# Optimization experiments

Hardware: AMD Instinct MI355X
Metric: run time of the kernel (lower is better)

## Reference

```python
import jax, jax.numpy as jnp
import numpy as np

B, L_I, L_H, L_Q, Hs, Ws, K, A = 256, 2, 150, 10, 128, 128, 40, 5


def _conv(x, w, pad):
    # NCHW conv, stride 1
    return jax.lax.conv_general_dilated(
        x, w, window_strides=(1, 1), padding=[(pad, pad), (pad, pad)],
        dimension_numbers=('NCHW', 'OIHW', 'NCHW'))


def setup_inputs() -> dict:
    key = jax.random.key(0)
    ks = jax.random.split(key, 8)
    return {
        'input_view': jax.random.normal(ks[0], (B, L_I, Hs, Ws), dtype=jnp.float32),
        'coords': jax.random.randint(ks[1], (B, 4), 0, Hs, dtype=jnp.int32),
        'h_w': jax.random.normal(ks[2], (L_H, L_I, 3, 3), dtype=jnp.float32) * 0.05,
        'h_b': jax.random.normal(ks[3], (L_H,), dtype=jnp.float32) * 0.05,
        'r_w': jax.random.normal(ks[4], (1, L_H, 1, 1), dtype=jnp.float32) * 0.05,
        'q_w': jax.random.normal(ks[5], (L_Q, 1, 3, 3), dtype=jnp.float32) * 0.05,
        'w': jax.random.normal(ks[6], (L_Q, 1, 3, 3), dtype=jnp.float32) * 0.05,
        'fc_w': jax.random.normal(ks[7], (A, L_Q), dtype=jnp.float32) * 0.05,
    }


def reference(input_view, coords, h_w, h_b, r_w, q_w, w, fc_w):
    # process_input: h = Conv3x3(input_view), r = Conv1x1(h), q0 = Conv3x3(r)
    h = _conv(input_view, h_w, pad=1) + h_b[None, :, None, None]
    r = _conv(h, r_w, pad=0)                       # [B,1,H,W] reward map
    q = _conv(r, q_w, pad=1)                       # [B,L_Q,H,W]
    v = jnp.max(q, axis=1, keepdims=True)          # [B,1,H,W]

    # value_iteration: k-1 sweeps of eval_q + channel max, then one final eval_q
    wq = jnp.concatenate([q_w, w], axis=1)         # [L_Q,2,3,3]

    def step(_, v):
        q_i = _conv(jnp.concatenate([r, v], axis=1), wq, pad=1)
        return jnp.max(q_i, axis=1, keepdims=True)

    v = jax.lax.fori_loop(0, K - 1, step, v)
    q = _conv(jnp.concatenate([r, v], axis=1), wq, pad=1)  # [B,L_Q,H,W]

    # get_action: gather q at agent state, then fc (no bias)
    sx, sy = coords[:, 0], coords[:, 1]
    q_out = q[jnp.arange(B), :, sx, sy]            # [B,L_Q]
    logits = q_out @ fc_w.T                        # [B,5]
    return logits
```

## Files before the change

kernel.cpp:

```cpp
#include <hip/hip_runtime.h>

#define NBATCH 256
#define LI 2
#define LH 150
#define LQ 10
#define HS 128
#define WSD 128
#define KIT 40
#define AOUT 5

#define LCOLS 132
#define LROWS 130
#define PLANE (LROWS * LCOLS)
#define LDS_DWORDS (2 * PLANE)

typedef float v2f __attribute__((ext_vector_type(2)));

__global__ void prep_weff(const float* __restrict__ h_w,
                          const float* __restrict__ h_b,
                          const float* __restrict__ r_w,
                          float* __restrict__ w_eff) {
  const int t = threadIdx.x;
  if (t < 18) {
    const int i = t / 9, k = t % 9;
    double s = 0.0;
    for (int h = 0; h < LH; ++h)
      s += (double)r_w[h] * (double)h_w[(h * LI + i) * 9 + k];
    w_eff[t] = (float)s;
  } else if (t == 18) {
    double s = 0.0;
    for (int h = 0; h < LH; ++h)
      s += (double)r_w[h] * (double)h_b[h];
    w_eff[18] = (float)s;
  }
}


#define LOAD_PROW(P, R, W)                                                   \
  {                                                                          \
    const float4 b_ = *reinterpret_cast<const float4*>((P) + (R) * LCOLS);   \
    const float2 c_ = *reinterpret_cast<const float2*>((P) + (R) * LCOLS + 4); \
    W[0] = (v2f){b_.x, b_.y};                                                \
    W[1] = (v2f){b_.z, b_.w};                                                \
    W[2] = (v2f){c_.x, c_.y};                                                \
  }

#define TAPROW(KY, WARR, K0, K1, K2)                                         \
    a0 = __builtin_elementwise_fma((v2f){(K0), (K0)}, WARR[KY][0], a0);      \
    a1 = __builtin_elementwise_fma((v2f){(K0), (K0)}, WARR[KY][1], a1);      \
    a0.x = __builtin_fmaf((K1), WARR[KY][0].y, a0.x);                        \
    a0.y = __builtin_fmaf((K1), WARR[KY][1].x, a0.y);                        \
    a1.x = __builtin_fmaf((K1), WARR[KY][1].y, a1.x);                        \
    a1.y = __builtin_fmaf((K1), WARR[KY][2].x, a1.y);                        \
    a0 = __builtin_elementwise_fma((v2f){(K2), (K2)}, WARR[KY][1], a0);      \
    a1 = __builtin_elementwise_fma((v2f){(K2), (K2)}, WARR[KY][2], a1);

#define VI_CH(QC, WC, MERGE)                                                 \
  {                                                                          \
    const float* qc = (QC);                                                  \
    const float* wc = (WC);                                                  \
    v2f a0 = (v2f){qc[0], qc[0]} * rw[0][0];                                 \
    v2f a1 = (v2f){qc[0], qc[0]} * rw[0][1];                                 \
    a0.x = __builtin_fmaf(qc[1], rw[0][0].y, a0.x);                          \
    a0.y = __builtin_fmaf(qc[1], rw[0][1].x, a0.y);                          \
    a1.x = __builtin_fmaf(qc[1], rw[0][1].y, a1.x);                          \
    a1.y = __builtin_fmaf(qc[1], rw[0][2].x, a1.y);                          \
    a0 = __builtin_elementwise_fma((v2f){qc[2], qc[2]}, rw[0][1], a0);       \
    a1 = __builtin_elementwise_fma((v2f){qc[2], qc[2]}, rw[0][2], a1);       \
    TAPROW(1, rw, qc[3], qc[4], qc[5])                                       \
    TAPROW(2, rw, qc[6], qc[7], qc[8])                                       \
    TAPROW(0, vw, wc[0], wc[1], wc[2])                                       \
    TAPROW(1, vw, wc[3], wc[4], wc[5])                                       \
    TAPROW(2, vw, wc[6], wc[7], wc[8])                                       \
    MERGE                                                                    \
  }

#define VI_ROW(DY)                                                           \
  {                                                                          \
    v2f o0, o1;                                                              \
    VI_CH(q_w, w_in, o0 = a0; o1 = a1;)                                      \
    _Pragma("unroll 3")                                                      \
    for (int c = 1; c < LQ; ++c) {                                           \
      VI_CH(q_w + c * 9, w_in + c * 9,                                       \
            o0 = __builtin_elementwise_max(o0, a0);                          \
            o1 = __builtin_elementwise_max(o1, a1);)                         \
    }                                                                        \
    outv[DY][0] = o0; outv[DY][1] = o1;                                      \
  }

#define WIN_SHIFT2(NEXTROW)                                                  \
  {                                                                          \
    _Pragma("unroll")                                                        \
    for (int j = 0; j < 3; ++j) {                                            \
      rw[0][j] = rw[1][j]; rw[1][j] = rw[2][j];                              \
      vw[0][j] = vw[1][j]; vw[1][j] = vw[2][j];                              \
    }                                                                        \
    LOAD_PROW(rp, (NEXTROW), rw[2])                                          \
    LOAD_PROW(vp, (NEXTROW), vw[2])                                          \
  }

#define R_ROW(DY)                                                            \
  {                                                                          \
    v2f a0 = (v2f){beff, beff};                                              \
    v2f a1 = a0;                                                             \
    TAPROW(0, rw, w_eff[0], w_eff[1], w_eff[2])                              \
    TAPROW(1, rw, w_eff[3], w_eff[4], w_eff[5])                              \
    TAPROW(2, rw, w_eff[6], w_eff[7], w_eff[8])                              \
    TAPROW(0, vw, w_eff[9], w_eff[10], w_eff[11])                            \
    TAPROW(1, vw, w_eff[12], w_eff[13], w_eff[14])                           \
    TAPROW(2, vw, w_eff[15], w_eff[16], w_eff[17])                           \
    racc[DY][0] = a0; racc[DY][1] = a1;                                      \
  }

__global__ __launch_bounds__(1024)
__attribute__((amdgpu_waves_per_eu(4, 4)))
void vin_main(const float* __restrict__ input,
              const int* __restrict__ coords,
              const float* __restrict__ q_w,
              const float* __restrict__ w_in,
              const float* __restrict__ fc_w,
              const float* __restrict__ w_eff,
              float* __restrict__ out) {
  extern __shared__ float lds[];
  float* rplane = lds;
  float* vplane = lds + PLANE;

  const int b = blockIdx.x;
  const int tid = threadIdx.x;
  const int ty = tid >> 5;
  const int tx = tid & 31;
  const int y0 = ty << 2;
  const int x0 = tx << 2;
  const int nb_base = y0 * LCOLS + x0;
  const int wrow0 = (y0 + 1) * LCOLS + x0;

  for (int i = tid; i < LDS_DWORDS; i += 1024) lds[i] = 0.0f;
  __syncthreads();

  const float* in0 = input + (size_t)b * (LI * HS * WSD);
  const float* in1 = in0 + HS * WSD;
  {
    const float4* in40 = (const float4*)in0;
    const float4* in41 = (const float4*)in1;
    for (int i = tid; i < HS * WSD / 4; i += 1024) {
      const int y = i >> 5, x4 = (i & 31) << 2;
      const float4 a = in40[i];
      const float4 c = in41[i];
      float* r_ = rplane + (y + 1) * LCOLS + x4;
      float* v_ = vplane + (y + 1) * LCOLS + x4;
      r_[1] = a.x; r_[2] = a.y; r_[3] = a.z; r_[4] = a.w;
      v_[1] = c.x; v_[2] = c.y; v_[3] = c.z; v_[4] = c.w;
    }
  }
  __syncthreads();

  {
    const float* rp = rplane + nb_base;
    const float* vp = vplane + nb_base;
    v2f rw[3][3], vw[3][3], racc[4][2];
    LOAD_PROW(rp, 0, rw[0]) LOAD_PROW(rp, 1, rw[1]) LOAD_PROW(rp, 2, rw[2])
    LOAD_PROW(vp, 0, vw[0]) LOAD_PROW(vp, 1, vw[1]) LOAD_PROW(vp, 2, vw[2])
    const float beff = w_eff[18];
    R_ROW(0) WIN_SHIFT2(3) R_ROW(1) WIN_SHIFT2(4) R_ROW(2) WIN_SHIFT2(5) R_ROW(3)
    __syncthreads();
#pragma unroll
    for (int dy = 0; dy < 4; ++dy) {
      float* r_ = rplane + wrow0 + dy * LCOLS;
      float* v_ = vplane + wrow0 + dy * LCOLS;
      r_[1] = racc[dy][0].x; r_[2] = racc[dy][0].y;
      r_[3] = racc[dy][1].x; r_[4] = racc[dy][1].y;
      v_[1] = 0.0f; v_[2] = 0.0f; v_[3] = 0.0f; v_[4] = 0.0f;
    }
  }
  __syncthreads();

#pragma unroll 1
  for (int it = 0; it < KIT; ++it) {
    const float* rp = rplane + nb_base;
    const float* vp = vplane + nb_base;
    v2f rw[3][3], vw[3][3], outv[4][2];
    LOAD_PROW(rp, 0, rw[0]) LOAD_PROW(rp, 1, rw[1]) LOAD_PROW(rp, 2, rw[2])
    LOAD_PROW(vp, 0, vw[0]) LOAD_PROW(vp, 1, vw[1]) LOAD_PROW(vp, 2, vw[2])
    VI_ROW(0) WIN_SHIFT2(3) VI_ROW(1) WIN_SHIFT2(4) VI_ROW(2) WIN_SHIFT2(5) VI_ROW(3)
    __syncthreads();
#pragma unroll
    for (int dy = 0; dy < 4; ++dy) {
      float* v_ = vplane + wrow0 + dy * LCOLS;
      v_[1] = outv[dy][0].x; v_[2] = outv[dy][0].y;
      v_[3] = outv[dy][1].x; v_[4] = outv[dy][1].y;
    }
    __syncthreads();
  }

  if (tid == 0) {
    const int sx = coords[b * 4 + 0];
    const int sy = coords[b * 4 + 1];
    float qv[LQ];
#pragma unroll 1
    for (int c = 0; c < LQ; ++c) {
      float s = 0.0f;
#pragma unroll
      for (int kk = 0; kk < 9; ++kk) {
        const int ky = kk / 3, kx = kk % 3;
        const int off = (sx + ky) * LCOLS + (sy + kx);
        s = __builtin_fmaf(q_w[c * 9 + kk], rplane[off],
            __builtin_fmaf(w_in[c * 9 + kk], vplane[off], s));
      }
      qv[c] = s;
    }
#pragma unroll 1
    for (int a = 0; a < AOUT; ++a) {
      float s = 0.0f;
#pragma unroll
      for (int c = 0; c < LQ; ++c)
        s = __builtin_fmaf(fc_w[a * LQ + c], qv[c], s);
      out[b * AOUT + a] = s;
    }
  }
}

extern "C" void kernel_launch(void* const* d_in, const int* in_sizes, int n_in,
                              void* d_out, int out_size, void* d_ws, size_t ws_size,
                              hipStream_t stream) {
  const float* input = (const float*)d_in[0];
  const int*   coords = (const int*)d_in[1];
  const float* h_w = (const float*)d_in[2];
  const float* h_b = (const float*)d_in[3];
  const float* r_w = (const float*)d_in[4];
  const float* q_w = (const float*)d_in[5];
  const float* w_in = (const float*)d_in[6];
  const float* fc_w = (const float*)d_in[7];
  float* out = (float*)d_out;
  float* w_eff = (float*)d_ws;

  const size_t smem = (size_t)LDS_DWORDS * sizeof(float);
  hipFuncSetAttribute(reinterpret_cast<const void*>(vin_main),
                      hipFuncAttributeMaxDynamicSharedMemorySize, (int)smem);

  prep_weff<<<1, 64, 0, stream>>>(h_w, h_b, r_w, w_eff);
  vin_main<<<NBATCH, 1024, smem, stream>>>(input, coords, q_w, w_in, fc_w, w_eff, out);
}
```

Baseline: 669.0 us.

## Move reward plane to global memory and ping-pong value planes in LDS

Adds a new kernel path that stores the fixed reward map r in a per-batch global workspace instead of LDS. This frees the second LDS plane so the value map can be double-buffered, letting each iteration write its output straight to the other buffer. That removes the register staging step and one __syncthreads per iteration. In exchange, every sweep reads the r neighborhood from global memory through the cache rather than from LDS. The old all-LDS kernel stays as a fallback when the workspace is too small.

Measured after the change: 654.4 us. 1.02x faster.

```diff
diff --git a/kernel.cpp b/kernel.cpp
--- a/kernel.cpp
+++ b/kernel.cpp
@@ -13,6 +13,9 @@
 #define LROWS 130
 #define PLANE (LROWS * LCOLS)
 #define LDS_DWORDS (2 * PLANE)
+
+#define WSOFF_RPLANES 64
+#define WS_NEED_BYTES ((size_t)(WSOFF_RPLANES + NBATCH * PLANE) * 4)
 
 typedef float v2f __attribute__((ext_vector_type(2)));
 
@@ -75,8 +78,7 @@
     MERGE                                                                    \
   }
 
-#define VI_ROW(DY)                                                           \
-  {                                                                          \
+#define VI_CHANNELS                                                          \
     v2f o0, o1;                                                              \
     VI_CH(q_w, w_in, o0 = a0; o1 = a1;)                                      \
     _Pragma("unroll 3")                                                      \
@@ -84,7 +86,18 @@
       VI_CH(q_w + c * 9, w_in + c * 9,                                       \
             o0 = __builtin_elementwise_max(o0, a0);                          \
             o1 = __builtin_elementwise_max(o1, a1);)                         \
-    }                                                                        \
+    }
+
+#define VI_ROW_G(DY)                                                         \
+  {                                                                          \
+    VI_CHANNELS                                                              \
+    float* w_ = wr + (DY) * LCOLS;                                           \
+    w_[1] = o0.x; w_[2] = o0.y; w_[3] = o1.x; w_[4] = o1.y;                  \
+  }
+
+#define VI_ROW_L(DY)                                                         \
+  {                                                                          \
+    VI_CHANNELS                                                              \
     outv[DY][0] = o0; outv[DY][1] = o1;                                      \
   }
 
@@ -114,13 +127,122 @@
 
 __global__ __launch_bounds__(1024)
 __attribute__((amdgpu_waves_per_eu(4, 4)))
-void vin_main(const float* __restrict__ input,
-              const int* __restrict__ coords,
-              const float* __restrict__ q_w,
-              const float* __restrict__ w_in,
-              const float* __restrict__ fc_w,
-              const float* __restrict__ w_eff,
-              float* __restrict__ out) {
+void vin_gr(const float* __restrict__ input,
+            const int* __restrict__ coords,
+            const float* __restrict__ q_w,
+            const float* __restrict__ w_in,
+            const float* __restrict__ fc_w,
+            float* __restrict__ ws,
+            float* __restrict__ out) {
+  extern __shared__ float lds[];
+  float* pA = lds;
+  float* pB = lds + PLANE;
+  const float* w_eff = ws;
+  float* g_r = ws + WSOFF_RPLANES + (size_t)blockIdx.x * PLANE;
+
+  const int b = blockIdx.x;
+  const int tid = threadIdx.x;
+  const int ty = tid >> 5;
+  const int tx = tid & 31;
+  const int y0 = ty << 2;
+  const int x0 = tx << 2;
+  const int nb_base = y0 * LCOLS + x0;
+  const int wrow0 = (y0 + 1) * LCOLS + x0;
+
+  for (int i = tid; i < LDS_DWORDS; i += 1024) lds[i] = 0.0f;
+  {
+    const float4 z4 = {0.0f, 0.0f, 0.0f, 0.0f};
+    float4* g4 = reinterpret_cast<float4*>(g_r);
+    for (int i = tid; i < PLANE / 4; i += 1024) g4[i] = z4;
+  }
+  __syncthreads();
+
+  const float* in0 = input + (size_t)b * (LI * HS * WSD);
+  const float* in1 = in0 + HS * WSD;
+  {
+    const float4* in40 = (const float4*)in0;
+    const float4* in41 = (const float4*)in1;
+    for (int i = tid; i < HS * WSD / 4; i += 1024) {
+      const int y = i >> 5, x4 = (i & 31) << 2;
+      const float4 a = in40[i];
+      const float4 c = in41[i];
+      float* r_ = pA + (y + 1) * LCOLS + x4;
+      float* v_ = pB + (y + 1) * LCOLS + x4;
+      r_[1] = a.x; r_[2] = a.y; r_[3] = a.z; r_[4] = a.w;
+      v_[1] = c.x; v_[2] = c.y; v_[3] = c.z; v_[4] = c.w;
+    }
+  }
+  __syncthreads();
+
+  {
+    const float* rp = pA + nb_base;
+    const float* vp = pB + nb_base;
+    v2f rw[3][3], vw[3][3], racc[4][2];
+    LOAD_PROW(rp, 0, rw[0]) LOAD_PROW(rp, 1, rw[1]) LOAD_PROW(rp, 2, rw[2])
+    LOAD_PROW(vp, 0, vw[0]) LOAD_PROW(vp, 1, vw[1]) LOAD_PROW(vp, 2, vw[2])
+    const float beff = w_eff[18];
+    R_ROW(0) WIN_SHIFT2(3) R_ROW(1) WIN_SHIFT2(4) R_ROW(2) WIN_SHIFT2(5) R_ROW(3)
+    __syncthreads();
+#pragma unroll
+    for (int dy = 0; dy < 4; ++dy) {
+      float* g_ = g_r + wrow0 + dy * LCOLS;
+      float* v_ = pA + wrow0 + dy * LCOLS;
+      g_[1] = racc[dy][0].x; g_[2] = racc[dy][0].y;
+      g_[3] = racc[dy][1].x; g_[4] = racc[dy][1].y;
+      v_[1] = 0.0f; v_[2] = 0.0f; v_[3] = 0.0f; v_[4] = 0.0f;
+    }
+  }
+  __syncthreads();
+
+  const float* grp = g_r + nb_base;
+#pragma unroll 1
+  for (int it = 0; it < KIT; ++it) {
+    const float* vp = lds + ((it & 1) ? PLANE : 0) + nb_base;
+    float* wr = lds + ((it & 1) ? 0 : PLANE) + wrow0;
+    const float* rp = grp;
+    v2f rw[3][3], vw[3][3];
+    LOAD_PROW(rp, 0, rw[0]) LOAD_PROW(rp, 1, rw[1]) LOAD_PROW(rp, 2, rw[2])
+    LOAD_PROW(vp, 0, vw[0]) LOAD_PROW(vp, 1, vw[1]) LOAD_PROW(vp, 2, vw[2])
+    VI_ROW_G(0) WIN_SHIFT2(3) VI_ROW_G(1) WIN_SHIFT2(4) VI_ROW_G(2) WIN_SHIFT2(5) VI_ROW_G(3)
+    __syncthreads();
+  }
+
+  if (tid == 0) {
+    const int sx = coords[b * 4 + 0];
+    const int sy = coords[b * 4 + 1];
+    float qv[LQ];
+#pragma unroll 1
+    for (int c = 0; c < LQ; ++c) {
+      float s = 0.0f;
+#pragma unroll
+      for (int kk = 0; kk < 9; ++kk) {
+        const int ky = kk / 3, kx = kk % 3;
+        const int off = (sx + ky) * LCOLS + (sy + kx);
+        s = __builtin_fmaf(q_w[c * 9 + kk], g_r[off],
+            __builtin_fmaf(w_in[c * 9 + kk], pA[off], s));
+      }
+      qv[c] = s;
+    }
+#pragma unroll 1
+    for (int a = 0; a < AOUT; ++a) {
+      float s = 0.0f;
+#pragma unroll
+      for (int c = 0; c < LQ; ++c)
+        s = __builtin_fmaf(fc_w[a * LQ + c], qv[c], s);
+      out[b * AOUT + a] = s;
+    }
+  }
+}
+
+__global__ __launch_bounds__(1024)
+__attribute__((amdgpu_waves_per_eu(4, 4)))
+void vin_lds(const float* __restrict__ input,
+             const int* __restrict__ coords,
+             const float* __restrict__ q_w,
+             const float* __restrict__ w_in,
+             const float* __restrict__ fc_w,
+             const float* __restrict__ w_eff,
+             float* __restrict__ out) {
   extern __shared__ float lds[];
   float* rplane = lds;
   float* vplane = lds + PLANE;
@@ -181,7 +303,7 @@
     v2f rw[3][3], vw[3][3], outv[4][2];
     LOAD_PROW(rp, 0, rw[0]) LOAD_PROW(rp, 1, rw[1]) LOAD_PROW(rp, 2, rw[2])
     LOAD_PROW(vp, 0, vw[0]) LOAD_PROW(vp, 1, vw[1]) LOAD_PROW(vp, 2, vw[2])
-    VI_ROW(0) WIN_SHIFT2(3) VI_ROW(1) WIN_SHIFT2(4) VI_ROW(2) WIN_SHIFT2(5) VI_ROW(3)
+    VI_ROW_L(0) WIN_SHIFT2(3) VI_ROW_L(1) WIN_SHIFT2(4) VI_ROW_L(2) WIN_SHIFT2(5) VI_ROW_L(3)
     __syncthreads();
 #pragma unroll
     for (int dy = 0; dy < 4; ++dy) {
@@ -231,12 +353,19 @@
   const float* w_in = (const float*)d_in[6];
   const float* fc_w = (const float*)d_in[7];
   float* out = (float*)d_out;
-  float* w_eff = (float*)d_ws;
+  float* ws = (float*)d_ws;
 
   const size_t smem = (size_t)LDS_DWORDS * sizeof(float);
-  hipFuncSetAttribute(reinterpret_cast<const void*>(vin_main),
-                      hipFuncAttributeMaxDynamicSharedMemorySize, (int)smem);
-
-  prep_weff<<<1, 64, 0, stream>>>(h_w, h_b, r_w, w_eff);
-  vin_main<<<NBATCH, 1024, smem, stream>>>(input, coords, q_w, w_in, fc_w, w_eff, out);
+
+  prep_weff<<<1, 64, 0, stream>>>(h_w, h_b, r_w, ws);
+
+  if (ws_size >= WS_NEED_BYTES) {
+    hipFuncSetAttribute(reinterpret_cast<const void*>(vin_gr),
+                        hipFuncAttributeMaxDynamicSharedMemorySize, (int)smem);
+    vin_gr<<<NBATCH, 1024, smem, stream>>>(input, coords, q_w, w_in, fc_w, ws, out);
+  } else {
+    hipFuncSetAttribute(reinterpret_cast<const void*>(vin_lds),
+                        hipFuncAttributeMaxDynamicSharedMemorySize, (int)smem);
+    vin_lds<<<NBATCH, 1024, smem, stream>>>(input, coords, q_w, w_in, fc_w, ws, out);
+  }
 }
```
